# Optimization experiments

Measured on AMD Instinct MI355X. Metric: run time of the kernel, lower is better.

The kernel has to match this reference:

```python
import jax, jax.numpy as jnp
import numpy as np

# Fixed production-scale dims (equal-size graphs -> no ragged padding needed)
B, NPG, C, H, L, FFN, NC = 16, 512, 128, 8, 4, 512, 4
D = C // H          # head dim = 16
T = NPG + 1         # +1 virtual graph token
EPG = 8192          # edges per graph (avg degree 16)
E = B * EPG


def _ln(x, g, b, eps=1e-5):
    m = x.mean(-1, keepdims=True)
    v = ((x - m) ** 2).mean(-1, keepdims=True)
    return (x - m) * jax.lax.rsqrt(v + eps) * g + b


def setup_inputs() -> dict:
    key = jax.random.key(0)
    ks = jax.random.split(key, 24)
    N = B * NPG
    node_feats = jax.random.normal(ks[0], (N, 3), jnp.float32)
    # intra-graph edges: local endpoints + per-graph node offset (matches batch_ptr math)
    local = jax.random.randint(ks[1], (2, B, EPG), 0, NPG)
    offs = (jnp.arange(B) * NPG)[None, :, None]
    edge_index = (local + offs).reshape(2, E)
    edge_attr = jax.random.randint(ks[2], (E,), 0, 10)

    def nrm(k, shape, scale=0.02):
        return jax.random.normal(k, shape, jnp.float32) * scale

    params = {
        "W_node": nrm(ks[3], (3, C), 0.3), "b_node": jnp.zeros((C,), jnp.float32),
        "graph_token": nrm(ks[4], (C,), 1.0),
        "edge_bias_table": nrm(ks[5], (11, H), 0.1).at[0].set(0.0),  # padding_idx=0
        "in_deg_emb": nrm(ks[6], (512, C)).at[0].set(0.0),           # padding_idx=0
        "out_deg_emb": nrm(ks[7], (512, C)).at[0].set(0.0),
        "vnode_bias": nrm(ks[8], (H,), 1.0),
        "Wq": nrm(ks[9], (L, C, C)), "bq": jnp.zeros((L, C), jnp.float32),
        "Wk": nrm(ks[10], (L, C, C)), "bk": jnp.zeros((L, C), jnp.float32),
        "Wv": nrm(ks[11], (L, C, C)), "bv": jnp.zeros((L, C), jnp.float32),
        "Wo": nrm(ks[12], (L, C, C)), "bo": jnp.zeros((L, C), jnp.float32),
        "ln1_g": jnp.ones((L, C), jnp.float32), "ln1_b": jnp.zeros((L, C), jnp.float32),
        "ln2_g": jnp.ones((L, C), jnp.float32), "ln2_b": jnp.zeros((L, C), jnp.float32),
        "W1": nrm(ks[13], (L, C, FFN)), "b1": jnp.zeros((L, FFN), jnp.float32),
        "W2": nrm(ks[14], (L, FFN, C)), "b2": jnp.zeros((L, C), jnp.float32),
        "normf_g": jnp.ones((C,), jnp.float32), "normf_b": jnp.zeros((C,), jnp.float32),
        "Wc1": nrm(ks[15], (C, C // 2)), "bc1": jnp.zeros((C // 2,), jnp.float32),
        "Wc2": nrm(ks[16], (C // 2, NC)), "bc2": jnp.zeros((NC,), jnp.float32),
    }
    return {"node_feats": node_feats, "edge_index": edge_index,
            "edge_attr": edge_attr, "num_graphs": B, **params}


def reference(node_feats, W_node, b_node, graph_token, edge_bias_table,
              in_deg_emb, out_deg_emb, vnode_bias,
              Wq, bq, Wk, bk, Wv, bv, Wo, bo,
              ln1_g, ln1_b, ln2_g, ln2_b, W1, b1, W2, b2,
              normf_g, normf_b, Wc1, bc1, Wc2, bc2,
              edge_index, edge_attr, num_graphs):
    N = node_feats.shape[0]
    npg = N // num_graphs
    t = npg + 1
    src, dst = edge_index[0], edge_index[1]
    # degree encoders (scatter_add of ones == segment_sum)
    in_deg = jnp.clip(jax.ops.segment_sum(jnp.ones_like(dst), dst, num_segments=N), 0, 511)
    out_deg = jnp.clip(jax.ops.segment_sum(jnp.ones_like(src), src, num_segments=N), 0, 511)
    x_enc = node_feats @ W_node + b_node + in_deg_emb[in_deg] + out_deg_emb[out_deg]
    # equal-size graphs with sorted batch ids -> padding loop is a reshape, mask all-False
    x = jnp.concatenate(
        [jnp.broadcast_to(graph_token, (num_graphs, 1, C)),
         x_enc.reshape(num_graphs, npg, C)], axis=1)  # [B, T, C]
    # attention bias: vnode row/col + scattered edge-attr embeddings
    bias = jnp.zeros((num_graphs, H, t, t), jnp.float32)
    bias = bias.at[:, :, 0, :].set(vnode_bias[None, :, None])
    bias = bias.at[:, :, :, 0].set(vnode_bias[None, :, None])
    eb = edge_bias_table[jnp.clip(edge_attr, 0, 9) + 1]  # [E, H]
    g = src // npg
    sl = src - g * npg + 1
    dl = dst - g * npg + 1
    bias = bias.at[g, :, sl, dl].add(eb)  # duplicate edges accumulate (scatter_add)
    scale = 1.0 / np.sqrt(D).astype(np.float32)
    for l in range(L):  # key_padding_mask is all-False here -> masked_fill is a no-op
        h = _ln(x, ln1_g[l], ln1_b[l])
        q = (h @ Wq[l] + bq[l]).reshape(num_graphs, t, H, D)
        k = (h @ Wk[l] + bk[l]).reshape(num_graphs, t, H, D)
        v = (h @ Wv[l] + bv[l]).reshape(num_graphs, t, H, D)
        scores = jnp.einsum('bthd,bshd->bhts', q, k) * scale + bias
        attn = jax.nn.softmax(scores, axis=-1)
        o = jnp.einsum('bhts,bshd->bthd', attn, v).reshape(num_graphs, t, C)
        x = x + o @ Wo[l] + bo[l]
        h2 = _ln(x, ln2_g[l], ln2_b[l])
        x = x + jax.nn.gelu(h2 @ W1[l] + b1[l], approximate=False) @ W2[l] + b2[l]
    x = _ln(x, normf_g, normf_b)
    gr = x[:, 0, :]  # virtual-node readout
    return jax.nn.gelu(gr @ Wc1 + bc1, approximate=False) @ Wc2 + bc2
```

## Files before the change

### kernel.cpp

```cpp
#include <hip/hip_runtime.h>
#include <hip/hip_bf16.h>

#define BB 16
#define NPG 512
#define CC 128
#define HH 8
#define LL 4
#define FFN 512
#define NCLS 4
#define DD 16
#define TT 513
#define EE 131072
#define NNODES 8192
#define ROWS (BB * TT)
#define ECAP 64
#define SP 544
#define BSTR 292

static constexpr size_t XROWS = (size_t)BB * TT;
static constexpr size_t XSZ   = XROWS * CC;
static constexpr size_t MIDSZ = XROWS * FFN;
static constexpr size_t VTSZ  = (size_t)BB * HH * DD * SP;

typedef unsigned short ushort_t;
typedef __attribute__((ext_vector_type(8))) short short8;
typedef __attribute__((ext_vector_type(4))) float floatx4;

__device__ __forceinline__ float gelu_exact(float v) {
    return 0.5f * v * (1.0f + erff(v * 0.70710678118654752440f));
}
__device__ __forceinline__ ushort_t f2bf(float f) {
    union { float f; unsigned u; } c; c.f = f;
    unsigned u = c.u;
    return (ushort_t)((u + 0x7FFFu + ((u >> 16) & 1u)) >> 16);
}

__global__ __launch_bounds__(256) void deg_csr_kernel(const int* __restrict__ ei,
                                                      const int* __restrict__ ea,
                                                      int* __restrict__ deg_in,
                                                      int* __restrict__ deg_out,
                                                      int* __restrict__ cnt,
                                                      int* __restrict__ ebuf) {
    int e = blockIdx.x * 256 + threadIdx.x;
    if (e >= EE) return;
    int src = ei[e], dst = ei[EE + e];
    atomicAdd(&deg_out[src], 1);
    atomicAdd(&deg_in[dst], 1);
    int g = src >> 9;
    int sl = src - (g << 9) + 1;
    int dl = dst - (g << 9) + 1;
    int a = ea[e];
    a = (a < 0) ? 0 : (a > 9 ? 9 : a);
    a += 1;
    int row = g * TT + sl;
    int pos = atomicAdd(&cnt[row], 1);
    if (pos < ECAP) ebuf[(size_t)row * ECAP + pos] = dl | (a << 16);
}

__global__ __launch_bounds__(256) void encode_kernel(const float* __restrict__ nf,
                                                     const float* __restrict__ Wn,
                                                     const float* __restrict__ bn,
                                                     const float* __restrict__ gt,
                                                     const float* __restrict__ ide,
                                                     const float* __restrict__ ode,
                                                     const int* __restrict__ deg_in,
                                                     const int* __restrict__ deg_out,
                                                     float* __restrict__ x) {
    int gid = blockIdx.x * 256 + threadIdx.x;
    if (gid >= (int)(XROWS * CC)) return;
    int c = gid & (CC - 1);
    int row = gid >> 7;
    int b = row / TT;
    int t = row - b * TT;
    float val;
    if (t == 0) {
        val = gt[c];
    } else {
        int i = b * NPG + t - 1;
        val = bn[c] + nf[i*3+0]*Wn[0*CC + c] + nf[i*3+1]*Wn[1*CC + c] + nf[i*3+2]*Wn[2*CC + c];
        int di = min(deg_in[i], 511);
        int dq = min(deg_out[i], 511);
        val += ide[(size_t)di * CC + c] + ode[(size_t)dq * CC + c];
    }
    x[(size_t)row * CC + c] = val;
}

struct TrDesc {
    const float* src[24];
    ushort_t*    dst[24];
    int          K[24];
    int          N[24];
};
__global__ __launch_bounds__(256) void tr_kernel(TrDesc d) {
    int z = blockIdx.z;
    int K = d.K[z], N = d.N[z];
    int tilesN = N >> 6;
    int ntile = (K >> 6) * tilesN;
    int tile = blockIdx.x;
    if (tile >= ntile) return;
    int k0 = (tile / tilesN) << 6;
    int n0 = (tile - (tile / tilesN) * tilesN) << 6;
    const float* src = d.src[z];
    ushort_t* dst = d.dst[z];
    __shared__ float t[64][65];
    int tid = threadIdx.x;
    int c = tid & 63, rb = tid >> 6;
    #pragma unroll
    for (int kk = 0; kk < 64; kk += 4)
        t[kk + rb][c] = src[(size_t)(k0 + kk + rb) * N + n0 + c];
    __syncthreads();
    #pragma unroll
    for (int nn = 0; nn < 64; nn += 4)
        dst[(size_t)(n0 + nn + rb) * K + k0 + c] = f2bf(t[c][nn + rb]);
}

__global__ __launch_bounds__(256) void ln_kernel(const float* __restrict__ in,
                                                 ushort_t* __restrict__ out,
                                                 const float* __restrict__ gg,
                                                 const float* __restrict__ bb) {
    int tid = threadIdx.x;
    int r2 = tid >> 7;
    int c = tid & 127;
    int row = blockIdx.x * 2 + r2;
    float v = in[(size_t)row * CC + c];
    float s1 = v, s2 = v * v;
    #pragma unroll
    for (int m = 32; m >= 1; m >>= 1) {
        s1 += __shfl_xor(s1, m, 64);
        s2 += __shfl_xor(s2, m, 64);
    }
    __shared__ float red[8];
    int w = tid >> 6;
    if ((tid & 63) == 0) { red[w*2] = s1; red[w*2+1] = s2; }
    __syncthreads();
    int wb = r2 * 4;
    float S1 = red[wb] + red[wb+2], S2 = red[wb+1] + red[wb+3];
    float mn = S1 * (1.0f/CC);
    float var = S2 * (1.0f/CC) - mn * mn;
    float rs = rsqrtf(var + 1e-5f);
    out[(size_t)row * CC + c] = f2bf((v - mn) * rs * gg[c] + bb[c]);
}

struct GP {
    const ushort_t* Wt[3];
    const float*    bias[3];
    float*          outF[3];
    ushort_t*       outB[3];
    const float*    lng[3];
    const float*    lnb[3];
    float           scl[3];
    int             md[3];
};
template<int K>
__global__ __launch_bounds__(256) void gemm_wave(const ushort_t* __restrict__ A, GP p,
                                                 const float* __restrict__ res,
                                                 int M, int N,
                                                 int mtiles, int ntiles) {
    int z = blockIdx.z;
    int wave = threadIdx.x >> 6;
    int wid = blockIdx.x * 4 + wave;
    int maxw = mtiles * ntiles;
    int widc = wid < maxw ? wid : maxw - 1;
    bool act = wid < maxw;
    int tm = widc / ntiles, tn = widc - tm * ntiles;
    int m0 = tm * 16, n0 = tn * 32;
    int lane = threadIdx.x & 63, lq = lane & 15, quad = lane >> 4;
    const short* Wt = (const short*)p.Wt[z];
    const short* Ab = (const short*)A;

    __shared__ float sred[4][16][2];

    size_t rowA  = (size_t)(m0 + lq) * K;
    size_t rowB0 = (size_t)(n0 + lq) * K;
    size_t rowB1 = (size_t)(n0 + 16 + lq) * K;

    floatx4 acc0 = {0.f, 0.f, 0.f, 0.f}, acc1 = acc0;
    #pragma unroll 4
    for (int k0 = 0; k0 < K; k0 += 32) {
        short8 af = *(const short8*)(Ab + rowA + k0 + quad * 8);
        short8 b0 = *(const short8*)(Wt + rowB0 + k0 + quad * 8);
        short8 b1 = *(const short8*)(Wt + rowB1 + k0 + quad * 8);
        acc0 = __builtin_amdgcn_mfma_f32_16x16x32_bf16(af, b0, acc0, 0, 0, 0);
        acc1 = __builtin_amdgcn_mfma_f32_16x16x32_bf16(af, b1, acc1, 0, 0, 0);
    }

    int mode = p.md[z];
    float scl = p.scl[z];
    float* outF = p.outF[z];
    ushort_t* outB = p.outB[z];
    int c0 = n0 + lq, c1 = n0 + 16 + lq;
    float bv0 = p.bias[z][c0], bv1 = p.bias[z][c1];

    if (mode == 4) {
        float vv0[4], vv1[4];
        #pragma unroll
        for (int rg = 0; rg < 4; ++rg) {
            int r = m0 + quad * 4 + rg;
            float a0 = acc0[rg] + bv0 + res[(size_t)r * N + c0];
            float a1 = acc1[rg] + bv1 + res[(size_t)r * N + c1];
            outF[(size_t)r * N + c0] = a0;
            outF[(size_t)r * N + c1] = a1;
            vv0[rg] = a0; vv1[rg] = a1;
        }
        #pragma unroll
        for (int rg = 0; rg < 4; ++rg) {
            float s1 = vv0[rg] + vv1[rg];
            float s2 = vv0[rg]*vv0[rg] + vv1[rg]*vv1[rg];
            #pragma unroll
            for (int m = 1; m < 16; m <<= 1) {
                s1 += __shfl_xor(s1, m, 64);
                s2 += __shfl_xor(s2, m, 64);
            }
            if (lq == 0) { sred[wave][quad*4+rg][0] = s1; sred[wave][quad*4+rg][1] = s2; }
        }
        __syncthreads();
        const float* gg = p.lng[z];
        const float* bb = p.lnb[z];
        float g0 = gg[c0], g1 = gg[c1], lb0 = bb[c0], lb1 = bb[c1];
        #pragma unroll
        for (int rg = 0; rg < 4; ++rg) {
            int row = quad * 4 + rg;
            float S1 = sred[0][row][0] + sred[1][row][0] + sred[2][row][0] + sred[3][row][0];
            float S2 = sred[0][row][1] + sred[1][row][1] + sred[2][row][1] + sred[3][row][1];
            float mn = S1 * (1.0f/CC);
            float var = S2 * (1.0f/CC) - mn * mn;
            float rs = rsqrtf(var + 1e-5f);
            int r = m0 + row;
            outB[(size_t)r * N + c0] = f2bf((vv0[rg] - mn) * rs * g0 + lb0);
            outB[(size_t)r * N + c1] = f2bf((vv1[rg] - mn) * rs * g1 + lb1);
        }
        return;
    }

    if (!act) return;
    #pragma unroll
    for (int rg = 0; rg < 4; ++rg) {
        int r = m0 + quad * 4 + rg;
        if (r >= M) continue;
        float a0 = acc0[rg] + bv0;
        float a1 = acc1[rg] + bv1;
        if (mode == 0) {
            outB[(size_t)r * N + c0] = f2bf(a0 * scl);
            outB[(size_t)r * N + c1] = f2bf(a1 * scl);
        } else if (mode == 1) {
            outF[(size_t)r * N + c0] = a0 + res[(size_t)r * N + c0];
            outF[(size_t)r * N + c1] = a1 + res[(size_t)r * N + c1];
        } else if (mode == 2) {
            outB[(size_t)r * N + c0] = f2bf(gelu_exact(a0));
            outB[(size_t)r * N + c1] = f2bf(gelu_exact(a1));
        } else {
            int bq = r / TT;
            int s = r - bq * TT;
            outB[((size_t)(bq * HH + (c0 >> 4)) * DD + (c0 & 15)) * SP + s] = f2bf(a0);
            outB[((size_t)(bq * HH + (c1 >> 4)) * DD + (c1 & 15)) * SP + s] = f2bf(a1);
        }
    }
}

__global__ __launch_bounds__(256) void attn_kernel(const ushort_t* __restrict__ qb,
                                                   const ushort_t* __restrict__ kb,
                                                   const ushort_t* __restrict__ vt,
                                                   const int* __restrict__ cnt,
                                                   const int* __restrict__ ebuf,
                                                   const float* __restrict__ ebt,
                                                   const float* __restrict__ vnode,
                                                   ushort_t* __restrict__ ob) {
    int bh = blockIdx.x;
    int qt = blockIdx.y;
    int b = bh >> 3, h = bh & (HH - 1);
    int tid = threadIdx.x;
    int wave = tid >> 6, lane = tid & 63, lq = lane & 15, quad = lane >> 4;

    __shared__ float arena[16 * BSTR];
    float* bstrip = arena;

    int qg = qt * 16 + lq;
    int qr = qg < TT ? qg : TT - 1;
    short8 qf = {0,0,0,0,0,0,0,0};
    if (quad < 2)
        qf = *(const short8*)(qb + ((size_t)(b * TT + qr)) * CC + h * DD + quad * 8);
    float vbh = vnode[h];
    int ql = tid >> 4, e0 = tid & 15;
    int qs = qt * 16 + ql;
    int crow = b * TT + (qs < TT ? qs : 0);
    int cn = (qs > 0 && qs < TT) ? min(cnt[crow], ECAP) : 0;

    const short* kbS = (const short*)kb;
    const short* vtS = (const short*)(vt + (size_t)bh * DD * SP);

    floatx4 oacc = {0.f, 0.f, 0.f, 0.f};
    float lsum = 0.f;

    #pragma unroll
    for (int ch = 0; ch < 2; ++ch) {
        int sp_lo = ch ? 9 : 0;
        int sp_hi = ch ? 17 : 9;
        int s_lo  = ch ? 288 : 0;
        int nrows = ch ? 256 : 288;

        int sp = sp_lo + wave;
        short8 af0 = {0,0,0,0,0,0,0,0}, af1 = af0, vf = af0;
        if (sp < sp_hi) {
            int st0 = sp * 2, st1 = sp * 2 + 1;
            int kr0 = min(b * TT + st0 * 16 + lq, (int)XROWS - 1);
            int kr1 = min(b * TT + st1 * 16 + lq, (int)XROWS - 1);
            if (quad < 2) {
                af0 = *(const short8*)(kbS + (size_t)kr0 * CC + h * DD + quad * 8);
                af1 = *(const short8*)(kbS + (size_t)kr1 * CC + h * DD + quad * 8);
            }
            vf = *(const short8*)(vtS + (size_t)lq * SP + sp * 32 + quad * 8);
        }

        for (int i = tid; i < 16 * BSTR / 4; i += 256)
            ((float4*)bstrip)[i] = make_float4(0.f, 0.f, 0.f, 0.f);
        __syncthreads();
        if (ch == 0 && tid < 16) {
            int q = qt * 16 + tid;
            if (q > 0 && q < TT) bstrip[tid * BSTR] = vbh;
        }
        for (int j = e0; j < cn; j += 16) {
            int e = ebuf[(size_t)crow * ECAP + j];
            int dl = e & 0xFFFF, a = e >> 16;
            int loc = dl - s_lo;
            if (loc >= 0 && loc < nrows)
                atomicAdd(&bstrip[ql * BSTR + loc], ebt[a * 8 + h]);
        }
        __syncthreads();

        for (; sp < sp_hi; sp += 4) {
            int spn = sp + 4;
            short8 nf0 = {0,0,0,0,0,0,0,0}, nf1 = nf0, nvf = nf0;
            if (spn < sp_hi) {
                int st0 = spn * 2, st1 = spn * 2 + 1;
                int kr0 = min(b * TT + st0 * 16 + lq, (int)XROWS - 1);
                int kr1 = min(b * TT + st1 * 16 + lq, (int)XROWS - 1);
                if (quad < 2) {
                    nf0 = *(const short8*)(kbS + (size_t)kr0 * CC + h * DD + quad * 8);
                    nf1 = *(const short8*)(kbS + (size_t)kr1 * CC + h * DD + quad * 8);
                }
                nvf = *(const short8*)(vtS + (size_t)lq * SP + spn * 32 + quad * 8);
            }

            unsigned pw[2][2];
            #pragma unroll
            for (int t = 0; t < 2; ++t) {
                int st = sp * 2 + t;
                floatx4 c = __builtin_amdgcn_mfma_f32_16x16x32_bf16(
                    t ? af1 : af0, qf, (floatx4){0.f, 0.f, 0.f, 0.f}, 0, 0, 0);
                float4 bi = *(const float4*)(bstrip + lq * BSTR + (st * 16 - s_lo) + quad * 4);
                float biv[4] = {bi.x, bi.y, bi.z, bi.w};
                float pr[4];
                #pragma unroll
                for (int rg = 0; rg < 4; ++rg) {
                    int s = st * 16 + quad * 4 + rg;
                    float p = 0.f;
                    if (s < TT) p = __expf(c[rg] + biv[rg]);
                    lsum += p;
                    pr[rg] = p;
                }
                pw[t][0] = (unsigned)f2bf(pr[0]) | ((unsigned)f2bf(pr[1]) << 16);
                pw[t][1] = (unsigned)f2bf(pr[2]) | ((unsigned)f2bf(pr[3]) << 16);
            }
            int srcA = lq + (((2 * quad) & 3) << 4);
            int srcB = lq + (((2 * quad + 1) & 3) << 4);
            int a00 = __shfl((int)pw[0][0], srcA, 64);
            int a01 = __shfl((int)pw[0][1], srcA, 64);
            int a10 = __shfl((int)pw[1][0], srcA, 64);
            int a11 = __shfl((int)pw[1][1], srcA, 64);
            int b00 = __shfl((int)pw[0][0], srcB, 64);
            int b01 = __shfl((int)pw[0][1], srcB, 64);
            int b10 = __shfl((int)pw[1][0], srcB, 64);
            int b11 = __shfl((int)pw[1][1], srcB, 64);
            union { int u[4]; short8 s8; } pu;
            bool lo = quad < 2;
            pu.u[0] = lo ? a00 : a10;
            pu.u[1] = lo ? a01 : a11;
            pu.u[2] = lo ? b00 : b10;
            pu.u[3] = lo ? b01 : b11;
            oacc = __builtin_amdgcn_mfma_f32_16x16x32_bf16(vf, pu.s8, oacc, 0, 0, 0);

            af0 = nf0; af1 = nf1; vf = nvf;
        }
        __syncthreads();
    }

    lsum += __shfl_xor(lsum, 16, 64);
    lsum += __shfl_xor(lsum, 32, 64);
    float* redw = arena;
    float* lsumS = arena + 1088;
    #pragma unroll
    for (int rg = 0; rg < 4; ++rg)
        redw[wave * 272 + (quad * 4 + rg) * 17 + lq] = oacc[rg];
    if (quad == 0) lsumS[wave * 16 + lq] = lsum;
    __syncthreads();

    {
        int q = tid >> 4, d = tid & 15;
        float o = 0.f, L = 0.f;
        #pragma unroll
        for (int w = 0; w < 4; ++w) {
            o += redw[w * 272 + d * 17 + q];
            L += lsumS[w * 16 + q];
        }
        int qq = qt * 16 + q;
        if (qq < TT)
            ob[((size_t)(b * TT + qq)) * CC + h * DD + d] = f2bf(o / L);
    }
}

__global__ __launch_bounds__(128) void head_kernel(const float* __restrict__ x,
                                                   const float* __restrict__ ng,
                                                   const float* __restrict__ nb,
                                                   const float* __restrict__ Wc1,
                                                   const float* __restrict__ bc1,
                                                   const float* __restrict__ Wc2,
                                                   const float* __restrict__ bc2,
                                                   float* __restrict__ out) {
    int b = blockIdx.x;
    int c = threadIdx.x;
    __shared__ float xfs[CC];
    __shared__ float c1s[64];
    __shared__ float red[4];

    float v = x[((size_t)b * TT) * CC + c];
    float s1 = v, s2 = v * v;
    #pragma unroll
    for (int m = 32; m >= 1; m >>= 1) {
        s1 += __shfl_xor(s1, m, 64);
        s2 += __shfl_xor(s2, m, 64);
    }
    int w = c >> 6;
    if ((c & 63) == 0) { red[w*2] = s1; red[w*2+1] = s2; }
    __syncthreads();
    float S1 = red[0] + red[2], S2 = red[1] + red[3];
    float mn = S1 * (1.0f/CC);
    float var = S2 * (1.0f/CC) - mn * mn;
    float rs = rsqrtf(var + 1e-5f);
    xfs[c] = (v - mn) * rs * ng[c] + nb[c];
    __syncthreads();
    if (c < 64) {
        float a = bc1[c];
        #pragma unroll 4
        for (int k = 0; k < CC; ++k) a = fmaf(xfs[k], Wc1[(size_t)k * 64 + c], a);
        c1s[c] = gelu_exact(a);
    }
    __syncthreads();
    if (c < NCLS) {
        float a = bc2[c];
        #pragma unroll 4
        for (int j = 0; j < 64; ++j) a = fmaf(c1s[j], Wc2[(size_t)j * NCLS + c], a);
        out[(size_t)b * NCLS + c] = a;
    }
}

extern "C" void kernel_launch(void* const* d_in, const int* in_sizes, int n_in,
                              void* d_out, int out_size, void* d_ws, size_t ws_size,
                              hipStream_t stream) {
    const float* node_feats = (const float*)d_in[0];
    const int*   edge_index = (const int*)d_in[1];
    const int*   edge_attr  = (const int*)d_in[2];
    const float* W_node  = (const float*)d_in[4];
    const float* b_node  = (const float*)d_in[5];
    const float* g_token = (const float*)d_in[6];
    const float* ebt     = (const float*)d_in[7];
    const float* ide     = (const float*)d_in[8];
    const float* ode     = (const float*)d_in[9];
    const float* vnode   = (const float*)d_in[10];
    const float* Wq = (const float*)d_in[11];
    const float* bq = (const float*)d_in[12];
    const float* Wk = (const float*)d_in[13];
    const float* bk = (const float*)d_in[14];
    const float* Wv = (const float*)d_in[15];
    const float* bv = (const float*)d_in[16];
    const float* Wo = (const float*)d_in[17];
    const float* bo = (const float*)d_in[18];
    const float* ln1g = (const float*)d_in[19];
    const float* ln1b = (const float*)d_in[20];
    const float* ln2g = (const float*)d_in[21];
    const float* ln2b = (const float*)d_in[22];
    const float* W1 = (const float*)d_in[23];
    const float* b1 = (const float*)d_in[24];
    const float* W2 = (const float*)d_in[25];
    const float* b2 = (const float*)d_in[26];
    const float* nfg = (const float*)d_in[27];
    const float* nfb = (const float*)d_in[28];
    const float* Wc1 = (const float*)d_in[29];
    const float* bc1 = (const float*)d_in[30];
    const float* Wc2 = (const float*)d_in[31];
    const float* bc2 = (const float*)d_in[32];
    float* out = (float*)d_out;

    char* base = (char*)d_ws;
    float* x      = (float*)base;     base += XSZ * 4;
    ushort_t* hbf = (ushort_t*)base;  base += XSZ * 2;
    ushort_t* qb  = (ushort_t*)base;  base += XSZ * 2;
    ushort_t* kb  = (ushort_t*)base;  base += XSZ * 2;
    ushort_t* vt  = (ushort_t*)base;  base += VTSZ * 2;
    ushort_t* obf = (ushort_t*)base;  base += XSZ * 2;
    ushort_t* mid = (ushort_t*)base;  base += MIDSZ * 2;
    ushort_t* wtqkvo = (ushort_t*)base; base += (size_t)16 * 16384 * 2;
    ushort_t* wt1 = (ushort_t*)base;  base += (size_t)4 * 65536 * 2;
    ushort_t* wt2 = (ushort_t*)base;  base += (size_t)4 * 65536 * 2;
    int* deg_in  = (int*)base;        base += NNODES * 4;
    int* deg_out = (int*)base;        base += NNODES * 4;
    int* cnt     = (int*)base;        base += (size_t)ROWS * 4;
    int* ebuf    = (int*)base;        base += (size_t)ROWS * ECAP * 4;

    hipMemsetAsync(deg_in, 0, (size_t)(2 * NNODES + ROWS) * 4, stream);
    deg_csr_kernel<<<EE / 256, 256, 0, stream>>>(edge_index, edge_attr,
                                                 deg_in, deg_out, cnt, ebuf);
    encode_kernel<<<(int)((XROWS * CC + 255) / 256), 256, 0, stream>>>(
        node_feats, W_node, b_node, g_token, ide, ode, deg_in, deg_out, x);

    TrDesc td;
    for (int l = 0; l < LL; ++l) {
        const float* srcs[4] = {Wq + (size_t)l*CC*CC, Wk + (size_t)l*CC*CC,
                                Wv + (size_t)l*CC*CC, Wo + (size_t)l*CC*CC};
        for (int k = 0; k < 4; ++k) {
            int slot = k * 4 + l;
            td.src[slot] = srcs[k];
            td.dst[slot] = wtqkvo + (size_t)slot * 16384;
            td.K[slot] = CC; td.N[slot] = CC;
        }
        td.src[16 + l] = W1 + (size_t)l*CC*FFN;
        td.dst[16 + l] = wt1 + (size_t)l*65536;
        td.K[16 + l] = CC; td.N[16 + l] = FFN;
        td.src[20 + l] = W2 + (size_t)l*FFN*CC;
        td.dst[20 + l] = wt2 + (size_t)l*65536;
        td.K[20 + l] = FFN; td.N[20 + l] = CC;
    }
    tr_kernel<<<dim3(16, 1, 24), 256, 0, stream>>>(td);

    const int MT16 = (int)(XROWS / 16);

    ln_kernel<<<(int)(XROWS / 2), 256, 0, stream>>>(x, hbf, ln1g, ln1b);

    for (int l = 0; l < LL; ++l) {
        GP pq = {};
        pq.Wt[0] = wtqkvo + (size_t)(0*4+l)*16384;
        pq.Wt[1] = wtqkvo + (size_t)(1*4+l)*16384;
        pq.Wt[2] = wtqkvo + (size_t)(2*4+l)*16384;
        pq.bias[0] = bq + l*CC; pq.bias[1] = bk + l*CC; pq.bias[2] = bv + l*CC;
        pq.outB[0] = qb; pq.outB[1] = kb; pq.outB[2] = vt;
        pq.scl[0] = 0.25f; pq.scl[1] = 1.0f; pq.scl[2] = 1.0f;
        pq.md[0] = 0; pq.md[1] = 0; pq.md[2] = 3;
        gemm_wave<CC><<<dim3(MT16, 1, 3), 256, 0, stream>>>(
            hbf, pq, nullptr, (int)XROWS, CC, MT16, 4);

        attn_kernel<<<dim3(BB*HH, 33), 256, 0, stream>>>(
            qb, kb, vt, cnt, ebuf, ebt, vnode, obf);

        GP po = {};
        po.Wt[0] = wtqkvo + (size_t)(3*4+l)*16384;
        po.bias[0] = bo + l*CC; po.outF[0] = x; po.outB[0] = hbf;
        po.lng[0] = ln2g + l*CC; po.lnb[0] = ln2b + l*CC;
        po.scl[0] = 1.0f; po.md[0] = 4;
        gemm_wave<CC><<<dim3(MT16, 1, 1), 256, 0, stream>>>(
            obf, po, x, (int)XROWS, CC, MT16, 4);

        GP p1 = {};
        p1.Wt[0] = wt1 + (size_t)l*65536;
        p1.bias[0] = b1 + l*FFN; p1.outB[0] = mid; p1.scl[0] = 1.0f; p1.md[0] = 2;
        gemm_wave<CC><<<dim3(MT16*4, 1, 1), 256, 0, stream>>>(
            hbf, p1, nullptr, (int)XROWS, FFN, MT16, 16);

        int ln_next = (l + 1) % LL;
        GP p2 = {};
        p2.Wt[0] = wt2 + (size_t)l*65536;
        p2.bias[0] = b2 + l*CC; p2.outF[0] = x; p2.outB[0] = hbf;
        p2.lng[0] = ln1g + ln_next*CC; p2.lnb[0] = ln1b + ln_next*CC;
        p2.scl[0] = 1.0f; p2.md[0] = 4;
        gemm_wave<FFN><<<dim3(MT16, 1, 1), 256, 0, stream>>>(
            mid, p2, x, (int)XROWS, CC, MT16, 4);
    }

    head_kernel<<<BB, 128, 0, stream>>>(x, nfg, nfb, Wc1, bc1, Wc2, bc2, out);
}
```

Measured before the change: 513.5 us.

## Fuse out-projection, LN2, FFN and next LN1 into one per-tile kernel

Replaces the three separate GEMM launches (Wo with residual+LN2, W1 with GELU, W2 with residual+LN1) by a single kernel in which each 16-row block keeps the normalized activations and the 512-wide FFN intermediate in swizzled shared memory. This removes the global round-trip of the FFN intermediate buffer and two kernel launches per layer. In exchange each block uses about 20KB of LDS and runs W1 as a 4-tile loop per wave, which may lower occupancy and parallelism relative to the wider W1 launch. The generic GEMM is trimmed to the Q/K/V modes only.

```diff
diff --git a/kernel.cpp b/kernel.cpp
--- a/kernel.cpp
+++ b/kernel.cpp
@@ -19,7 +19,6 @@
 
 static constexpr size_t XROWS = (size_t)BB * TT;
 static constexpr size_t XSZ   = XROWS * CC;
-static constexpr size_t MIDSZ = XROWS * FFN;
 static constexpr size_t VTSZ  = (size_t)BB * HH * DD * SP;
 
 typedef unsigned short ushort_t;
@@ -33,6 +32,10 @@
     union { float f; unsigned u; } c; c.f = f;
     unsigned u = c.u;
     return (ushort_t)((u + 0x7FFFu + ((u >> 16) & 1u)) >> 16);
+}
+__device__ __forceinline__ int swz(int row, int col, int stride) {
+    int kb = col >> 3;
+    return row * stride + (((kb ^ (row & 7)) << 3) | (col & 7));
 }
 
 __global__ __launch_bounds__(256) void deg_csr_kernel(const int* __restrict__ ei,
@@ -144,31 +147,24 @@
 struct GP {
     const ushort_t* Wt[3];
     const float*    bias[3];
-    float*          outF[3];
     ushort_t*       outB[3];
-    const float*    lng[3];
-    const float*    lnb[3];
     float           scl[3];
     int             md[3];
 };
 template<int K>
 __global__ __launch_bounds__(256) void gemm_wave(const ushort_t* __restrict__ A, GP p,
-                                                 const float* __restrict__ res,
                                                  int M, int N,
                                                  int mtiles, int ntiles) {
     int z = blockIdx.z;
     int wave = threadIdx.x >> 6;
     int wid = blockIdx.x * 4 + wave;
     int maxw = mtiles * ntiles;
-    int widc = wid < maxw ? wid : maxw - 1;
-    bool act = wid < maxw;
-    int tm = widc / ntiles, tn = widc - tm * ntiles;
+    if (wid >= maxw) return;
+    int tm = wid / ntiles, tn = wid - tm * ntiles;
     int m0 = tm * 16, n0 = tn * 32;
     int lane = threadIdx.x & 63, lq = lane & 15, quad = lane >> 4;
     const short* Wt = (const short*)p.Wt[z];
     const short* Ab = (const short*)A;
-
-    __shared__ float sred[4][16][2];
 
     size_t rowA  = (size_t)(m0 + lq) * K;
     size_t rowB0 = (size_t)(n0 + lq) * K;
@@ -186,21 +182,72 @@
 
     int mode = p.md[z];
     float scl = p.scl[z];
-    float* outF = p.outF[z];
     ushort_t* outB = p.outB[z];
     int c0 = n0 + lq, c1 = n0 + 16 + lq;
     float bv0 = p.bias[z][c0], bv1 = p.bias[z][c1];
 
-    if (mode == 4) {
-        float vv0[4], vv1[4];
+    #pragma unroll
+    for (int rg = 0; rg < 4; ++rg) {
+        int r = m0 + quad * 4 + rg;
+        float a0 = acc0[rg] + bv0;
+        float a1 = acc1[rg] + bv1;
+        if (mode == 0) {
+            outB[(size_t)r * N + c0] = f2bf(a0 * scl);
+            outB[(size_t)r * N + c1] = f2bf(a1 * scl);
+        } else {
+            int bq = r / TT;
+            int s = r - bq * TT;
+            outB[((size_t)(bq * HH + (c0 >> 4)) * DD + (c0 & 15)) * SP + s] = f2bf(a0);
+            outB[((size_t)(bq * HH + (c1 >> 4)) * DD + (c1 & 15)) * SP + s] = f2bf(a1);
+        }
+    }
+}
+
+__global__ __launch_bounds__(256) void mega_kernel(const ushort_t* __restrict__ obf,
+                                                   const ushort_t* __restrict__ WtO,
+                                                   const float* __restrict__ bo_,
+                                                   const float* __restrict__ ln2g_,
+                                                   const float* __restrict__ ln2b_,
+                                                   const ushort_t* __restrict__ Wt1_,
+                                                   const float* __restrict__ b1_,
+                                                   const ushort_t* __restrict__ Wt2_,
+                                                   const float* __restrict__ b2_,
+                                                   const float* __restrict__ ln1g_,
+                                                   const float* __restrict__ ln1b_,
+                                                   float* __restrict__ x_,
+                                                   ushort_t* __restrict__ hbf_) {
+    int m0 = blockIdx.x * 16;
+    int tid = threadIdx.x;
+    int wave = tid >> 6, lane = tid & 63, lq = lane & 15, quad = lane >> 4;
+
+    __shared__ ushort_t hs[16 * 128];
+    __shared__ ushort_t ms[16 * 512];
+    __shared__ float sred[4][16][2];
+
+    int n0 = wave * 32;
+    int c0 = n0 + lq, c1 = n0 + 16 + lq;
+    float vv0[4], vv1[4];
+
+    {
+        const short* Ab = (const short*)obf;
+        const short* W = (const short*)WtO;
+        size_t rowA = (size_t)(m0 + lq) * CC;
+        size_t rB0 = (size_t)(n0 + lq) * CC, rB1 = (size_t)(n0 + 16 + lq) * CC;
+        floatx4 a0 = {0.f,0.f,0.f,0.f}, a1 = a0;
+        #pragma unroll
+        for (int k0 = 0; k0 < CC; k0 += 32) {
+            short8 af = *(const short8*)(Ab + rowA + k0 + quad * 8);
+            short8 b0 = *(const short8*)(W + rB0 + k0 + quad * 8);
+            short8 b1 = *(const short8*)(W + rB1 + k0 + quad * 8);
+            a0 = __builtin_amdgcn_mfma_f32_16x16x32_bf16(af, b0, a0, 0, 0, 0);
+            a1 = __builtin_amdgcn_mfma_f32_16x16x32_bf16(af, b1, a1, 0, 0, 0);
+        }
+        float bv0 = bo_[c0], bv1 = bo_[c1];
         #pragma unroll
         for (int rg = 0; rg < 4; ++rg) {
             int r = m0 + quad * 4 + rg;
-            float a0 = acc0[rg] + bv0 + res[(size_t)r * N + c0];
-            float a1 = acc1[rg] + bv1 + res[(size_t)r * N + c1];
-            outF[(size_t)r * N + c0] = a0;
-            outF[(size_t)r * N + c1] = a1;
-            vv0[rg] = a0; vv1[rg] = a1;
+            vv0[rg] = a0[rg] + bv0 + x_[(size_t)r * CC + c0];
+            vv1[rg] = a1[rg] + bv1 + x_[(size_t)r * CC + c1];
         }
         #pragma unroll
         for (int rg = 0; rg < 4; ++rg) {
@@ -214,9 +261,84 @@
             if (lq == 0) { sred[wave][quad*4+rg][0] = s1; sred[wave][quad*4+rg][1] = s2; }
         }
         __syncthreads();
-        const float* gg = p.lng[z];
-        const float* bb = p.lnb[z];
-        float g0 = gg[c0], g1 = gg[c1], lb0 = bb[c0], lb1 = bb[c1];
+        float g0 = ln2g_[c0], g1 = ln2g_[c1], lb0 = ln2b_[c0], lb1 = ln2b_[c1];
+        #pragma unroll
+        for (int rg = 0; rg < 4; ++rg) {
+            int row = quad * 4 + rg;
+            float S1 = sred[0][row][0] + sred[1][row][0] + sred[2][row][0] + sred[3][row][0];
+            float S2 = sred[0][row][1] + sred[1][row][1] + sred[2][row][1] + sred[3][row][1];
+            float mn = S1 * (1.0f/CC);
+            float var = S2 * (1.0f/CC) - mn * mn;
+            float rs = rsqrtf(var + 1e-5f);
+            hs[swz(row, c0, 128)] = f2bf((vv0[rg] - mn) * rs * g0 + lb0);
+            hs[swz(row, c1, 128)] = f2bf((vv1[rg] - mn) * rs * g1 + lb1);
+        }
+    }
+    __syncthreads();
+
+    {
+        const short* hsS = (const short*)hs;
+        const short* W = (const short*)Wt1_;
+        #pragma unroll
+        for (int nt = 0; nt < 4; ++nt) {
+            int n = wave * 128 + nt * 32;
+            size_t rB0 = (size_t)(n + lq) * CC, rB1 = (size_t)(n + 16 + lq) * CC;
+            floatx4 a0 = {0.f,0.f,0.f,0.f}, a1 = a0;
+            #pragma unroll
+            for (int k0 = 0; k0 < CC; k0 += 32) {
+                short8 af = *(const short8*)(hsS + swz(lq, k0 + quad * 8, 128));
+                short8 b0 = *(const short8*)(W + rB0 + k0 + quad * 8);
+                short8 b1 = *(const short8*)(W + rB1 + k0 + quad * 8);
+                a0 = __builtin_amdgcn_mfma_f32_16x16x32_bf16(af, b0, a0, 0, 0, 0);
+                a1 = __builtin_amdgcn_mfma_f32_16x16x32_bf16(af, b1, a1, 0, 0, 0);
+            }
+            float bb0 = b1_[n + lq], bb1 = b1_[n + 16 + lq];
+            #pragma unroll
+            for (int rg = 0; rg < 4; ++rg) {
+                int row = quad * 4 + rg;
+                ms[swz(row, n + lq, 512)]      = f2bf(gelu_exact(a0[rg] + bb0));
+                ms[swz(row, n + 16 + lq, 512)] = f2bf(gelu_exact(a1[rg] + bb1));
+            }
+        }
+    }
+    __syncthreads();
+
+    {
+        const short* msS = (const short*)ms;
+        const short* W = (const short*)Wt2_;
+        size_t rB0 = (size_t)(n0 + lq) * FFN, rB1 = (size_t)(n0 + 16 + lq) * FFN;
+        floatx4 a0 = {0.f,0.f,0.f,0.f}, a1 = a0;
+        #pragma unroll 4
+        for (int k0 = 0; k0 < FFN; k0 += 32) {
+            short8 af = *(const short8*)(msS + swz(lq, k0 + quad * 8, 512));
+            short8 b0 = *(const short8*)(W + rB0 + k0 + quad * 8);
+            short8 b1 = *(const short8*)(W + rB1 + k0 + quad * 8);
+            a0 = __builtin_amdgcn_mfma_f32_16x16x32_bf16(af, b0, a0, 0, 0, 0);
+            a1 = __builtin_amdgcn_mfma_f32_16x16x32_bf16(af, b1, a1, 0, 0, 0);
+        }
+        float bv0 = b2_[c0], bv1 = b2_[c1];
+        float w0[4], w1[4];
+        #pragma unroll
+        for (int rg = 0; rg < 4; ++rg) {
+            int r = m0 + quad * 4 + rg;
+            w0[rg] = a0[rg] + bv0 + vv0[rg];
+            w1[rg] = a1[rg] + bv1 + vv1[rg];
+            x_[(size_t)r * CC + c0] = w0[rg];
+            x_[(size_t)r * CC + c1] = w1[rg];
+        }
+        #pragma unroll
+        for (int rg = 0; rg < 4; ++rg) {
+            float s1 = w0[rg] + w1[rg];
+            float s2 = w0[rg]*w0[rg] + w1[rg]*w1[rg];
+            #pragma unroll
+            for (int m = 1; m < 16; m <<= 1) {
+                s1 += __shfl_xor(s1, m, 64);
+                s2 += __shfl_xor(s2, m, 64);
+            }
+            if (lq == 0) { sred[wave][quad*4+rg][0] = s1; sred[wave][quad*4+rg][1] = s2; }
+        }
+        __syncthreads();
+        float g0 = ln1g_[c0], g1 = ln1g_[c1], lb0 = ln1b_[c0], lb1 = ln1b_[c1];
         #pragma unroll
         for (int rg = 0; rg < 4; ++rg) {
             int row = quad * 4 + rg;
@@ -226,33 +348,8 @@
             float var = S2 * (1.0f/CC) - mn * mn;
             float rs = rsqrtf(var + 1e-5f);
             int r = m0 + row;
-            outB[(size_t)r * N + c0] = f2bf((vv0[rg] - mn) * rs * g0 + lb0);
-            outB[(size_t)r * N + c1] = f2bf((vv1[rg] - mn) * rs * g1 + lb1);
-        }
-        return;
-    }
-
-    if (!act) return;
-    #pragma unroll
-    for (int rg = 0; rg < 4; ++rg) {
-        int r = m0 + quad * 4 + rg;
-        if (r >= M) continue;
-        float a0 = acc0[rg] + bv0;
-        float a1 = acc1[rg] + bv1;
-        if (mode == 0) {
-            outB[(size_t)r * N + c0] = f2bf(a0 * scl);
-            outB[(size_t)r * N + c1] = f2bf(a1 * scl);
-        } else if (mode == 1) {
-            outF[(size_t)r * N + c0] = a0 + res[(size_t)r * N + c0];
-            outF[(size_t)r * N + c1] = a1 + res[(size_t)r * N + c1];
-        } else if (mode == 2) {
-            outB[(size_t)r * N + c0] = f2bf(gelu_exact(a0));
-            outB[(size_t)r * N + c1] = f2bf(gelu_exact(a1));
-        } else {
-            int bq = r / TT;
-            int s = r - bq * TT;
-            outB[((size_t)(bq * HH + (c0 >> 4)) * DD + (c0 & 15)) * SP + s] = f2bf(a0);
-            outB[((size_t)(bq * HH + (c1 >> 4)) * DD + (c1 & 15)) * SP + s] = f2bf(a1);
+            hbf_[(size_t)r * CC + c0] = f2bf((w0[rg] - mn) * rs * g0 + lb0);
+            hbf_[(size_t)r * CC + c1] = f2bf((w1[rg] - mn) * rs * g1 + lb1);
         }
     }
 }
@@ -497,7 +594,6 @@
     ushort_t* kb  = (ushort_t*)base;  base += XSZ * 2;
     ushort_t* vt  = (ushort_t*)base;  base += VTSZ * 2;
     ushort_t* obf = (ushort_t*)base;  base += XSZ * 2;
-    ushort_t* mid = (ushort_t*)base;  base += MIDSZ * 2;
     ushort_t* wtqkvo = (ushort_t*)base; base += (size_t)16 * 16384 * 2;
     ushort_t* wt1 = (ushort_t*)base;  base += (size_t)4 * 65536 * 2;
     ushort_t* wt2 = (ushort_t*)base;  base += (size_t)4 * 65536 * 2;
@@ -545,33 +641,20 @@
         pq.scl[0] = 0.25f; pq.scl[1] = 1.0f; pq.scl[2] = 1.0f;
         pq.md[0] = 0; pq.md[1] = 0; pq.md[2] = 3;
         gemm_wave<CC><<<dim3(MT16, 1, 3), 256, 0, stream>>>(
-            hbf, pq, nullptr, (int)XROWS, CC, MT16, 4);
+            hbf, pq, (int)XROWS, CC, MT16, 4);
 
         attn_kernel<<<dim3(BB*HH, 33), 256, 0, stream>>>(
             qb, kb, vt, cnt, ebuf, ebt, vnode, obf);
 
-        GP po = {};
-        po.Wt[0] = wtqkvo + (size_t)(3*4+l)*16384;
-        po.bias[0] = bo + l*CC; po.outF[0] = x; po.outB[0] = hbf;
-        po.lng[0] = ln2g + l*CC; po.lnb[0] = ln2b + l*CC;
-        po.scl[0] = 1.0f; po.md[0] = 4;
-        gemm_wave<CC><<<dim3(MT16, 1, 1), 256, 0, stream>>>(
-            obf, po, x, (int)XROWS, CC, MT16, 4);
-
-        GP p1 = {};
-        p1.Wt[0] = wt1 + (size_t)l*65536;
-        p1.bias[0] = b1 + l*FFN; p1.outB[0] = mid; p1.scl[0] = 1.0f; p1.md[0] = 2;
-        gemm_wave<CC><<<dim3(MT16*4, 1, 1), 256, 0, stream>>>(
-            hbf, p1, nullptr, (int)XROWS, FFN, MT16, 16);
-
         int ln_next = (l + 1) % LL;
-        GP p2 = {};
-        p2.Wt[0] = wt2 + (size_t)l*65536;
-        p2.bias[0] = b2 + l*CC; p2.outF[0] = x; p2.outB[0] = hbf;
-        p2.lng[0] = ln1g + ln_next*CC; p2.lnb[0] = ln1b + ln_next*CC;
-        p2.scl[0] = 1.0f; p2.md[0] = 4;
-        gemm_wave<FFN><<<dim3(MT16, 1, 1), 256, 0, stream>>>(
-            mid, p2, x, (int)XROWS, CC, MT16, 4);
+        mega_kernel<<<MT16, 256, 0, stream>>>(
+            obf,
+            wtqkvo + (size_t)(3*4+l)*16384, bo + l*CC,
+            ln2g + l*CC, ln2b + l*CC,
+            wt1 + (size_t)l*65536, b1 + l*FFN,
+            wt2 + (size_t)l*65536, b2 + l*CC,
+            ln1g + ln_next*CC, ln1b + ln_next*CC,
+            x, hbf);
     }
 
     head_kernel<<<BB, 128, 0, stream>>>(x, nfg, nfb, Wc1, bc1, Wc2, bc2, out);
```

After: 452.2 us. 11.9% less time.
